# Kernel tuning notes

Measured on AMD Instinct MI355X. Metric: run time of the kernel, lower is better.

Reference implementation:

```python
import jax, jax.numpy as jnp
from jax import lax
import numpy as np

B, T, CIN, COUT = 64, 16384, 8, 8
N_A, N_B = 3, 3


def setup_inputs() -> dict:
    key = jax.random.key(0)
    k1, k2, k3, k4 = jax.random.split(key, 4)
    u = jax.random.normal(k1, (B, T, CIN), dtype=jnp.float32)
    x0 = jax.random.normal(k2, (B, N_A, COUT), dtype=jnp.float32)
    # Small AR coefficients so the IIR recursion is stable (sum |a_k| < 1).
    a_coeff = jax.random.uniform(k3, (N_A, COUT), dtype=jnp.float32,
                                 minval=-0.15, maxval=0.15)
    b_coeff = jax.random.normal(k4, (N_B + 1, CIN, COUT), dtype=jnp.float32)
    return {"u": u, "x0": x0, "a_coeff": a_coeff, "b_coeff": b_coeff}


def reference(u, x0, a_coeff, b_coeff):
    n_b = b_coeff.shape[0] - 1
    n_a = a_coeff.shape[0]
    # Causal FIR part: pad front of time axis, valid conv, channels_last.
    u_pad = jnp.pad(u, ((0, 0), (n_b, 0), (0, 0)))
    b_u = lax.conv_general_dilated(
        u_pad, b_coeff, window_strides=(1,), padding='VALID',
        dimension_numbers=('NWC', 'WIO', 'NWC'))  # [B, T, COUT]
    if n_a == 0:
        return b_u
    # Fold initial condition x0 into the first time step.
    first = b_u[:, 0, :] + jnp.einsum('to,bto->bo', jnp.flip(a_coeff, axis=0), x0)
    b_u = jnp.concatenate([first[:, None, :], b_u[:, 1:, :]], axis=1)
    # Stack n_a shifted copies (prepend tail of x0): [B, n_a, T, COUT]
    stacked = jnp.stack(
        [jnp.concatenate([x0[:, n_a - idx:, :], b_u[:, idx:, :]], axis=1)
         for idx in range(n_a)], axis=1)
    # Companion-style transition: a_ss[s, n, o] = a_coeff[n, o] if n >= s else 0.
    a_ss = jnp.stack(
        [jnp.pad(a_coeff[idx:, :], ((idx, 0), (0, 0))) for idx in range(n_a)],
        axis=0)  # [n_a, n_a, COUT]

    def a_apply(x, y):
        return jnp.einsum('sno,bnto->bsto', a_ss, x) + y

    y = lax.associative_scan(a_apply, stacked, axis=2)
    return y[:, 0, :, :]  # [B, T, COUT]
```

## Files before the change

kernel.cpp:

```cpp
#include <hip/hip_runtime.h>

#define T_SZ   16384
#define CIN    8
#define COUT   8
#define NPART  16
#define PART_T 1024
#define NCHUNK 32
#define CHT    32

struct V3 { float x, y, z; };
__device__ __forceinline__ V3 mkv3(float a, float b, float c) { V3 r; r.x=a; r.y=b; r.z=c; return r; }
__device__ __forceinline__ V3 vadd3(V3 a, V3 b) { return mkv3(a.x+b.x, a.y+b.y, a.z+b.z); }
__device__ __forceinline__ V3 vfma3(V3 acc, float s, V3 w) {
  return mkv3(fmaf(s, w.x, acc.x), fmaf(s, w.y, acc.y), fmaf(s, w.z, acc.z));
}
__device__ __forceinline__ V3 aappf(float a0, float a1, float a2, V3 v) {
  float t2 = a2 * v.z;
  float t1 = fmaf(a1, v.y, t2);
  return mkv3(fmaf(a0, v.x, t1), t1, t2);
}
__device__ __forceinline__ V3 comb(float a0, float a1, float a2, V3 l, V3 r) {
  return vadd3(aappf(a0, a1, a2, l), r);
}

struct Row { float4 lo, hi; };
__device__ __forceinline__ Row ldrow(const float* p) {
  Row r; r.lo = *(const float4*)p; r.hi = *(const float4*)(p + 4); return r;
}
__device__ __forceinline__ Row zrow() { Row r; r.lo = make_float4(0.f,0.f,0.f,0.f); r.hi = r.lo; return r; }
__device__ __forceinline__ float rdot(const Row& r, const float* w) {
  float s = r.lo.x * w[0];
  s = fmaf(r.lo.y, w[1], s); s = fmaf(r.lo.z, w[2], s); s = fmaf(r.lo.w, w[3], s);
  s = fmaf(r.hi.x, w[4], s); s = fmaf(r.hi.y, w[5], s); s = fmaf(r.hi.z, w[6], s);
  s = fmaf(r.hi.w, w[7], s);
  return s;
}

struct Pre {
  float bv[CHT];
  V3 e0, e1, E5;
  float a0, a1, a2;
  int o, c, p, b, t0;
};

__device__ __forceinline__ void preamble(
    Pre& P, const float* __restrict__ u, const float* __restrict__ x0,
    const float* __restrict__ ac, const float* __restrict__ bc)
{
  const int j = threadIdx.x;
  P.o = j & 7;  P.c = j >> 3;
  P.p = blockIdx.x & 15;  P.b = blockIdx.x >> 4;
  const int o = P.o;
  P.a0 = ac[0*COUT + o];  P.a1 = ac[1*COUT + o];  P.a2 = ac[2*COUT + o];
  const float a0 = P.a0, a1 = P.a1, a2 = P.a2;

  float w0[8], w1[8], w2[8], w3[8];
#pragma unroll
  for (int i = 0; i < 8; ++i) {
    w0[i] = bc[(0*CIN + i)*COUT + o];
    w1[i] = bc[(1*CIN + i)*COUT + o];
    w2[i] = bc[(2*CIN + i)*COUT + o];
    w3[i] = bc[(3*CIN + i)*COUT + o];
  }

  const float* ub = u + (size_t)P.b * T_SZ * CIN;
  P.t0 = P.p * PART_T + P.c * CHT;
  const int t0 = P.t0;

  {
    Row ra, rb, rc;
    if (t0 == 0) { ra = zrow(); rb = zrow(); rc = zrow(); }
    else {
      ra = ldrow(ub + (size_t)(t0 - 3) * CIN);
      rb = ldrow(ub + (size_t)(t0 - 2) * CIN);
      rc = ldrow(ub + (size_t)(t0 - 1) * CIN);
    }
#pragma unroll
    for (int r = 0; r < CHT; ++r) {
      Row rd = ldrow(ub + (size_t)(t0 + r) * CIN);
      P.bv[r] = rdot(ra, w0) + rdot(rb, w1) + rdot(rc, w2) + rdot(rd, w3);
      ra = rb; rb = rc; rc = rd;
    }
  }

  P.e0 = mkv3(0,0,0);  P.e1 = mkv3(0,0,0);
  if (t0 == 0) {
    float x00 = x0[((size_t)P.b*3 + 0)*COUT + o];
    float x01 = x0[((size_t)P.b*3 + 1)*COUT + o];
    float x02 = x0[((size_t)P.b*3 + 2)*COUT + o];
    float first = P.bv[0] + a2*x00 + a1*x01 + a0*x02;
    P.e0 = mkv3(first, x02, x01);
    P.e1 = mkv3(P.bv[1], P.bv[1], x02);
  }

  V3 gt[6];
  gt[0] = mkv3(1.f,1.f,1.f);
#pragma unroll
  for (int k = 1; k <= 5; ++k) gt[k] = aappf(a0,a1,a2, gt[k-1]);
  V3 acc;
  if (t0 == 0) {
    V3 q0 = P.e0, q1 = P.e1;
#pragma unroll
    for (int k = 0; k < 5; ++k) q0 = aappf(a0,a1,a2, q0);
#pragma unroll
    for (int k = 0; k < 4; ++k) q1 = aappf(a0,a1,a2, q1);
    acc = vadd3(q0, q1);
#pragma unroll
    for (int r = 2; r < CHT; ++r) acc = vfma3(acc, P.bv[r], gt[5 - __popc(r)]);
  } else {
    acc = mkv3(0,0,0);
#pragma unroll
    for (int r = 0; r < CHT; ++r) acc = vfma3(acc, P.bv[r], gt[5 - __popc(r)]);
  }
  P.E5 = acc;
}

__global__ __launch_bounds__(256) void ldtf_p1(
    const float* __restrict__ u, const float* __restrict__ x0,
    const float* __restrict__ ac, const float* __restrict__ bc,
    float* __restrict__ ws)
{
  __shared__ V3 s_E5[NCHUNK*8];
  __shared__ V3 s_tr[30*8];

  Pre P;
  preamble(P, u, x0, ac, bc);
  const int j = threadIdx.x, o = P.o;
  const float a0 = P.a0, a1 = P.a1, a2 = P.a2;

  s_E5[P.c*8 + o] = P.E5;
  __syncthreads();
  if (j < 128) { int i = j >> 3; s_tr[i*8+o]      = comb(a0,a1,a2, s_E5[(2*i)*8+o],    s_E5[(2*i+1)*8+o]); }
  __syncthreads();
  if (j < 64)  { int i = j >> 3; s_tr[(16+i)*8+o] = comb(a0,a1,a2, s_tr[(2*i)*8+o],    s_tr[(2*i+1)*8+o]); }
  __syncthreads();
  if (j < 32)  { int i = j >> 3; s_tr[(24+i)*8+o] = comb(a0,a1,a2, s_tr[(16+2*i)*8+o], s_tr[(16+2*i+1)*8+o]); }
  __syncthreads();
  if (j < 16)  { int i = j >> 3; s_tr[(28+i)*8+o] = comb(a0,a1,a2, s_tr[(24+2*i)*8+o], s_tr[(24+2*i+1)*8+o]); }
  __syncthreads();
  if (j < 8) {
    V3 rt = comb(a0,a1,a2, s_tr[28*8+o], s_tr[29*8+o]);
    float* wp = ws + ((size_t)(P.b*NPART + P.p)*8 + o)*3;
    wp[0] = rt.x; wp[1] = rt.y; wp[2] = rt.z;
  }
}

#define POOL_FLOATS 8448

__global__ __launch_bounds__(256) void ldtf_p2(
    const float* __restrict__ u, const float* __restrict__ x0,
    const float* __restrict__ ac, const float* __restrict__ bc,
    float* __restrict__ out, const float* __restrict__ ws)
{
  __shared__ __align__(16) float s_pool[POOL_FLOATS];
  V3* s_E5 = (V3*)s_pool;
  V3* s_tr = (V3*)s_pool + 256;
  V3* s_mt = (V3*)s_pool + 496;
  float* s_out = s_pool;

  Pre P;
  preamble(P, u, x0, ac, bc);
  const int j = threadIdx.x, o = P.o, c = P.c, p = P.p, b = P.b;
  const float a0 = P.a0, a1 = P.a1, a2 = P.a2;

  s_E5[c*8 + o] = P.E5;
  if (j < 128) {
    int c2 = j >> 3;
    const float* wp = ws + ((size_t)(b*NPART + c2)*8 + o)*3;
    s_mt[c2*8+o] = mkv3(wp[0], wp[1], wp[2]);
  }
  __syncthreads();

  if (j < 128) { int i = j >> 3; s_tr[i*8+o]      = comb(a0,a1,a2, s_E5[(2*i)*8+o],    s_E5[(2*i+1)*8+o]); }
  else         { int i = (j-128) >> 3; if (i < 8) s_mt[(16+i)*8+o] = comb(a0,a1,a2, s_mt[(2*i)*8+o], s_mt[(2*i+1)*8+o]); }
  __syncthreads();
  if (j < 64)  { int i = j >> 3; s_tr[(16+i)*8+o] = comb(a0,a1,a2, s_tr[(2*i)*8+o],    s_tr[(2*i+1)*8+o]); }
  else if (j >= 128) { int i = (j-128) >> 3; if (i < 4) s_mt[(24+i)*8+o] = comb(a0,a1,a2, s_mt[(16+2*i)*8+o], s_mt[(16+2*i+1)*8+o]); }
  __syncthreads();
  if (j < 32)  { int i = j >> 3; s_tr[(24+i)*8+o] = comb(a0,a1,a2, s_tr[(16+2*i)*8+o], s_tr[(16+2*i+1)*8+o]); }
  else if (j >= 128) { int i = (j-128) >> 3; if (i < 2) s_mt[(28+i)*8+o] = comb(a0,a1,a2, s_mt[(24+2*i)*8+o], s_mt[(24+2*i+1)*8+o]); }
  __syncthreads();
  if (j < 16)  { int i = j >> 3; s_tr[(28+i)*8+o] = comb(a0,a1,a2, s_tr[(24+2*i)*8+o], s_tr[(24+2*i+1)*8+o]); }
  __syncthreads();

  V3 sig = mkv3(0,0,0);
  if ((p >> 3) & 1) sig = comb(a0,a1,a2, sig, s_mt[(28 + (p>>3) - 1)*8 + o]);
  if ((p >> 2) & 1) sig = comb(a0,a1,a2, sig, s_mt[(24 + (p>>2) - 1)*8 + o]);
  if ((p >> 1) & 1) sig = comb(a0,a1,a2, sig, s_mt[(16 + (p>>1) - 1)*8 + o]);
  if (p & 1)        sig = comb(a0,a1,a2, sig, s_mt[(p - 1)*8 + o]);
  if ((c >> 4) & 1) sig = comb(a0,a1,a2, sig, s_tr[(28 + (c>>4) - 1)*8 + o]);
  if ((c >> 3) & 1) sig = comb(a0,a1,a2, sig, s_tr[(24 + (c>>3) - 1)*8 + o]);
  if ((c >> 2) & 1) sig = comb(a0,a1,a2, sig, s_tr[(16 + (c>>2) - 1)*8 + o]);
  if ((c >> 1) & 1) sig = comb(a0,a1,a2, sig, s_tr[((c>>1) - 1)*8 + o]);
  if (c & 1)        sig = comb(a0,a1,a2, sig, s_E5[(c - 1)*8 + o]);

  V3 tau;
  {
    int q = p + 1;
    if (q == 16) tau = comb(a0,a1,a2, s_mt[28*8+o], s_mt[29*8+o]);
    else {
      tau = mkv3(0,0,0);
      if ((q >> 3) & 1) tau = comb(a0,a1,a2, tau, s_mt[(28 + (q>>3) - 1)*8 + o]);
      if ((q >> 2) & 1) tau = comb(a0,a1,a2, tau, s_mt[(24 + (q>>2) - 1)*8 + o]);
      if ((q >> 1) & 1) tau = comb(a0,a1,a2, tau, s_mt[(16 + (q>>1) - 1)*8 + o]);
      if (q & 1)        tau = comb(a0,a1,a2, tau, s_mt[(q - 1)*8 + o]);
    }
  }
  __syncthreads();

  if (c >= 1) s_out[(c - 1)*264 + 31*8 + o] = sig.x;
  if (c == NCHUNK - 1) s_out[31*264 + 31*8 + o] = tau.x;

  {
    V3 st[5];
#pragma unroll
    for (int r = 0; r < CHT - 1; ++r) {
      V3 v = mkv3(P.bv[r], P.bv[r], P.bv[r]);
      if (P.t0 == 0) { if (r == 0) v = P.e0; if (r == 1) v = P.e1; }
      if (r & 1)          v = comb(a0,a1,a2, st[0], v);
      if ((r & 3) == 3)   v = comb(a0,a1,a2, st[1], v);
      if ((r & 7) == 7)   v = comb(a0,a1,a2, st[2], v);
      if ((r & 15) == 15) v = comb(a0,a1,a2, st[3], v);
      const int lvl = (r & 1) ? (((r & 3) == 3) ? (((r & 7) == 7) ? (((r & 15) == 15) ? 4 : 3) : 2) : 1) : 0;
      st[lvl] = v;
      const int i = r + 1;
      V3 acc = sig;
      if (i & 16) acc = comb(a0,a1,a2, acc, st[4]);
      if (i & 8)  acc = comb(a0,a1,a2, acc, st[3]);
      if (i & 4)  acc = comb(a0,a1,a2, acc, st[2]);
      if (i & 2)  acc = comb(a0,a1,a2, acc, st[1]);
      if (i & 1)  acc = comb(a0,a1,a2, acc, st[0]);
      s_out[c*264 + r*8 + o] = acc.x;
    }
  }
  __syncthreads();

  float* og = out + ((size_t)b * T_SZ + (size_t)p * PART_T) * COUT;
#pragma unroll
  for (int it = 0; it < 8; ++it) {
    int f = (it * 256 + j) * 4;
    float4 v = *(const float4*)&s_out[(f >> 8) * 264 + (f & 255)];
    *(float4*)&og[f] = v;
  }
}

extern "C" void kernel_launch(void* const* d_in, const int* in_sizes, int n_in,
                              void* d_out, int out_size, void* d_ws, size_t ws_size,
                              hipStream_t stream) {
  const float* u  = (const float*)d_in[0];
  const float* x0 = (const float*)d_in[1];
  const float* ac = (const float*)d_in[2];
  const float* bc = (const float*)d_in[3];
  float* outp = (float*)d_out;
  float* wsp  = (float*)d_ws;
  (void)ws_size; (void)in_sizes; (void)n_in; (void)out_size;
  const int grid = 64 * NPART;
  ldtf_p1<<<dim3(grid), dim3(256), 0, stream>>>(u, x0, ac, bc, wsp);
  ldtf_p2<<<dim3(grid), dim3(256), 0, stream>>>(u, x0, ac, bc, outp, wsp);
}
```

Measured before the change: 131.9 us.

## Fuse two-pass scan into one persistent kernel with grid-wide atomic barrier

```diff
diff --git a/kernel.cpp b/kernel.cpp
--- a/kernel.cpp
+++ b/kernel.cpp
@@ -7,6 +7,8 @@
 #define PART_T 1024
 #define NCHUNK 32
 #define CHT    32
+#define GRID_BLOCKS (64 * NPART)
+#define BAR_OFFSET_BYTES (1 << 17)
 
 struct V3 { float x, y, z; };
 __device__ __forceinline__ V3 mkv3(float a, float b, float c) { V3 r; r.x=a; r.y=b; r.z=c; return r; }
@@ -244,6 +246,124 @@
   }
 }
 
+__global__ __launch_bounds__(256) void ldtf_fused(
+    const float* __restrict__ u, const float* __restrict__ x0,
+    const float* __restrict__ ac, const float* __restrict__ bc,
+    float* __restrict__ out, float* __restrict__ ws,
+    unsigned int* __restrict__ bar)
+{
+  __shared__ __align__(16) float s_pool[POOL_FLOATS];
+  V3* s_E5 = (V3*)s_pool;
+  V3* s_tr = (V3*)s_pool + 256;
+  V3* s_mt = (V3*)s_pool + 496;
+  float* s_out = s_pool;
+
+  Pre P;
+  preamble(P, u, x0, ac, bc);
+  const int j = threadIdx.x, o = P.o, c = P.c, p = P.p, b = P.b;
+  const float a0 = P.a0, a1 = P.a1, a2 = P.a2;
+
+  s_E5[c*8 + o] = P.E5;
+  __syncthreads();
+  if (j < 128) { int i = j >> 3; s_tr[i*8+o]      = comb(a0,a1,a2, s_E5[(2*i)*8+o],    s_E5[(2*i+1)*8+o]); }
+  __syncthreads();
+  if (j < 64)  { int i = j >> 3; s_tr[(16+i)*8+o] = comb(a0,a1,a2, s_tr[(2*i)*8+o],    s_tr[(2*i+1)*8+o]); }
+  __syncthreads();
+  if (j < 32)  { int i = j >> 3; s_tr[(24+i)*8+o] = comb(a0,a1,a2, s_tr[(16+2*i)*8+o], s_tr[(16+2*i+1)*8+o]); }
+  __syncthreads();
+  if (j < 16)  { int i = j >> 3; s_tr[(28+i)*8+o] = comb(a0,a1,a2, s_tr[(24+2*i)*8+o], s_tr[(24+2*i+1)*8+o]); }
+  __syncthreads();
+  if (j < 8) {
+    V3 rt = comb(a0,a1,a2, s_tr[28*8+o], s_tr[29*8+o]);
+    float* wp = ws + ((size_t)(b*NPART + p)*8 + o)*3;
+    wp[0] = rt.x; wp[1] = rt.y; wp[2] = rt.z;
+  }
+  __syncthreads();
+  if (j == 0) {
+    __threadfence();
+    atomicAdd(bar, 1u);
+    while (__hip_atomic_load(bar, __ATOMIC_ACQUIRE, __HIP_MEMORY_SCOPE_AGENT)
+           < (unsigned)GRID_BLOCKS) {
+      __builtin_amdgcn_s_sleep(2);
+    }
+  }
+  __syncthreads();
+  __threadfence();
+
+  if (j < 128) {
+    int c2 = j >> 3;
+    const float* wp = ws + ((size_t)(b*NPART + c2)*8 + o)*3;
+    s_mt[c2*8+o] = mkv3(wp[0], wp[1], wp[2]);
+  }
+  __syncthreads();
+  if (j < 64) { int i = j >> 3; s_mt[(16+i)*8+o] = comb(a0,a1,a2, s_mt[(2*i)*8+o],    s_mt[(2*i+1)*8+o]); }
+  __syncthreads();
+  if (j < 32) { int i = j >> 3; s_mt[(24+i)*8+o] = comb(a0,a1,a2, s_mt[(16+2*i)*8+o], s_mt[(16+2*i+1)*8+o]); }
+  __syncthreads();
+  if (j < 16) { int i = j >> 3; s_mt[(28+i)*8+o] = comb(a0,a1,a2, s_mt[(24+2*i)*8+o], s_mt[(24+2*i+1)*8+o]); }
+  __syncthreads();
+
+  V3 sig = mkv3(0,0,0);
+  if ((p >> 3) & 1) sig = comb(a0,a1,a2, sig, s_mt[(28 + (p>>3) - 1)*8 + o]);
+  if ((p >> 2) & 1) sig = comb(a0,a1,a2, sig, s_mt[(24 + (p>>2) - 1)*8 + o]);
+  if ((p >> 1) & 1) sig = comb(a0,a1,a2, sig, s_mt[(16 + (p>>1) - 1)*8 + o]);
+  if (p & 1)        sig = comb(a0,a1,a2, sig, s_mt[(p - 1)*8 + o]);
+  if ((c >> 4) & 1) sig = comb(a0,a1,a2, sig, s_tr[(28 + (c>>4) - 1)*8 + o]);
+  if ((c >> 3) & 1) sig = comb(a0,a1,a2, sig, s_tr[(24 + (c>>3) - 1)*8 + o]);
+  if ((c >> 2) & 1) sig = comb(a0,a1,a2, sig, s_tr[(16 + (c>>2) - 1)*8 + o]);
+  if ((c >> 1) & 1) sig = comb(a0,a1,a2, sig, s_tr[((c>>1) - 1)*8 + o]);
+  if (c & 1)        sig = comb(a0,a1,a2, sig, s_E5[(c - 1)*8 + o]);
+
+  V3 tau;
+  {
+    int q = p + 1;
+    if (q == 16) tau = comb(a0,a1,a2, s_mt[28*8+o], s_mt[29*8+o]);
+    else {
+      tau = mkv3(0,0,0);
+      if ((q >> 3) & 1) tau = comb(a0,a1,a2, tau, s_mt[(28 + (q>>3) - 1)*8 + o]);
+      if ((q >> 2) & 1) tau = comb(a0,a1,a2, tau, s_mt[(24 + (q>>2) - 1)*8 + o]);
+      if ((q >> 1) & 1) tau = comb(a0,a1,a2, tau, s_mt[(16 + (q>>1) - 1)*8 + o]);
+      if (q & 1)        tau = comb(a0,a1,a2, tau, s_mt[(q - 1)*8 + o]);
+    }
+  }
+  __syncthreads();
+
+  if (c >= 1) s_out[(c - 1)*264 + 31*8 + o] = sig.x;
+  if (c == NCHUNK - 1) s_out[31*264 + 31*8 + o] = tau.x;
+
+  {
+    V3 st[5];
+#pragma unroll
+    for (int r = 0; r < CHT - 1; ++r) {
+      V3 v = mkv3(P.bv[r], P.bv[r], P.bv[r]);
+      if (P.t0 == 0) { if (r == 0) v = P.e0; if (r == 1) v = P.e1; }
+      if (r & 1)          v = comb(a0,a1,a2, st[0], v);
+      if ((r & 3) == 3)   v = comb(a0,a1,a2, st[1], v);
+      if ((r & 7) == 7)   v = comb(a0,a1,a2, st[2], v);
+      if ((r & 15) == 15) v = comb(a0,a1,a2, st[3], v);
+      const int lvl = (r & 1) ? (((r & 3) == 3) ? (((r & 7) == 7) ? (((r & 15) == 15) ? 4 : 3) : 2) : 1) : 0;
+      st[lvl] = v;
+      const int i = r + 1;
+      V3 acc = sig;
+      if (i & 16) acc = comb(a0,a1,a2, acc, st[4]);
+      if (i & 8)  acc = comb(a0,a1,a2, acc, st[3]);
+      if (i & 4)  acc = comb(a0,a1,a2, acc, st[2]);
+      if (i & 2)  acc = comb(a0,a1,a2, acc, st[1]);
+      if (i & 1)  acc = comb(a0,a1,a2, acc, st[0]);
+      s_out[c*264 + r*8 + o] = acc.x;
+    }
+  }
+  __syncthreads();
+
+  float* og = out + ((size_t)b * T_SZ + (size_t)p * PART_T) * COUT;
+#pragma unroll
+  for (int it = 0; it < 8; ++it) {
+    int f = (it * 256 + j) * 4;
+    float4 v = *(const float4*)&s_out[(f >> 8) * 264 + (f & 255)];
+    *(float4*)&og[f] = v;
+  }
+}
+
 extern "C" void kernel_launch(void* const* d_in, const int* in_sizes, int n_in,
                               void* d_out, int out_size, void* d_ws, size_t ws_size,
                               hipStream_t stream) {
@@ -253,8 +373,25 @@
   const float* bc = (const float*)d_in[3];
   float* outp = (float*)d_out;
   float* wsp  = (float*)d_ws;
-  (void)ws_size; (void)in_sizes; (void)n_in; (void)out_size;
-  const int grid = 64 * NPART;
-  ldtf_p1<<<dim3(grid), dim3(256), 0, stream>>>(u, x0, ac, bc, wsp);
-  ldtf_p2<<<dim3(grid), dim3(256), 0, stream>>>(u, x0, ac, bc, outp, wsp);
-}
+  (void)in_sizes; (void)n_in; (void)out_size;
+
+  static int fused_ok = -1;
+  if (fused_ok < 0) {
+    int nb = 0, ncu = 0, dev = 0;
+    hipGetDevice(&dev);
+    hipDeviceProp_t prop;
+    if (hipGetDeviceProperties(&prop, dev) == hipSuccess) ncu = prop.multiProcessorCount;
+    if (hipOccupancyMaxActiveBlocksPerMultiprocessor(&nb, ldtf_fused, 256, 0) != hipSuccess) nb = 0;
+    fused_ok = (nb > 0 && ncu > 0 && (long)nb * ncu >= GRID_BLOCKS &&
+                ws_size >= (size_t)BAR_OFFSET_BYTES + 16) ? 1 : 0;
+  }
+
+  if (fused_ok == 1) {
+    unsigned int* bar = (unsigned int*)((char*)d_ws + BAR_OFFSET_BYTES);
+    hipMemsetAsync(bar, 0, sizeof(unsigned int), stream);
+    ldtf_fused<<<dim3(GRID_BLOCKS), dim3(256), 0, stream>>>(u, x0, ac, bc, outp, wsp, bar);
+  } else {
+    ldtf_p1<<<dim3(GRID_BLOCKS), dim3(256), 0, stream>>>(u, x0, ac, bc, wsp);
+    ldtf_p2<<<dim3(GRID_BLOCKS), dim3(256), 0, stream>>>(u, x0, ac, bc, outp, wsp);
+  }
+}
```

Result: no change. 131.5 us (-0.3%).
